# Kernel optimization log

Hardware: AMD Instinct MI355X
Metric: run time of the kernel (lower is better)

## Reference

```python
import jax, jax.numpy as jnp
import numpy as np
from jax import lax

NUM_HEADS = 4
OUT_DIM = 384
HEAD_DIM = 96
STRIDE_Q = 2
STRIDE_KV = 2
EPS = 1e-6
SCALE = HEAD_DIM ** -0.5


def _layernorm(x, g, b):
    m = jnp.mean(x, axis=-1, keepdims=True)
    v = jnp.mean((x - m) ** 2, axis=-1, keepdims=True)
    return (x - m) * lax.rsqrt(v + EPS) * g + b


def _pool(x, w, h, wd, stride):
    # x: [B, nh, N, hd] -> depthwise conv stride-s -> [B, nh, oh*ow, hd]
    B, nh, N, hd = x.shape
    x = x.reshape(B * nh, h, wd, hd).transpose(0, 3, 1, 2)  # NCHW
    y = lax.conv_general_dilated(x, w, (stride, stride), ((1, 1), (1, 1)),
                                 feature_group_count=hd)
    oh, ow = y.shape[2], y.shape[3]
    y = y.reshape(B, nh, hd, oh * ow).transpose(0, 1, 3, 2)
    return y, (oh, ow)


def _add_rel_pos(attn, q, q_size, k_size, rel_h, rel_w):
    qh, qw = q_size
    kh, kw = k_size
    B, nh, _, hd = q.shape
    qhr = max(kh / qh, 1.0); khr = max(qh / kh, 1.0)
    dh = (jnp.arange(qh)[:, None] * qhr - jnp.arange(kh)[None, :] * khr
          + (kh - 1) * khr).astype(jnp.int32)
    qwr = max(kw / qw, 1.0); kwr = max(qw / kw, 1.0)
    dw = (jnp.arange(qw)[:, None] * qwr - jnp.arange(kw)[None, :] * kwr
          + (kw - 1) * kwr).astype(jnp.int32)
    Reh = rel_h[dh]  # [qh, kh, hd]
    Rew = rel_w[dw]  # [qw, kw, hd]
    qr = q.reshape(B, nh, qh, qw, hd)
    eh = jnp.einsum('byhwc,hkc->byhwk', qr, Reh)
    ew = jnp.einsum('byhwc,wkc->byhwk', qr, Rew)
    a = attn.reshape(B, nh, qh, qw, kh, kw) + eh[..., :, None] + ew[..., None, :]
    return a.reshape(B, nh, qh * qw, kh * kw)


def setup_inputs() -> dict:
    key = jax.random.key(0)
    ks = jax.random.split(key, 8)
    B, N, IN_DIM = 16, 3136, 192
    return {
        'hidden_states': jax.random.normal(ks[0], (B, N, IN_DIM), jnp.float32),
        'qkv_w': jax.random.normal(ks[1], (IN_DIM, 3 * OUT_DIM), jnp.float32) * 0.02,
        'qkv_b': jax.random.normal(ks[2], (3 * OUT_DIM,), jnp.float32) * 0.02,
        'pool_q_w': jax.random.normal(ks[3], (HEAD_DIM, 1, 3, 3), jnp.float32) * 0.1,
        'pool_k_w': jax.random.normal(ks[4], (HEAD_DIM, 1, 3, 3), jnp.float32) * 0.1,
        'pool_v_w': jax.random.normal(ks[5], (HEAD_DIM, 1, 3, 3), jnp.float32) * 0.1,
        'ln_q_g': jnp.ones((HEAD_DIM,), jnp.float32),
        'ln_q_b': jnp.zeros((HEAD_DIM,), jnp.float32),
        'ln_k_g': jnp.ones((HEAD_DIM,), jnp.float32),
        'ln_k_b': jnp.zeros((HEAD_DIM,), jnp.float32),
        'ln_v_g': jnp.ones((HEAD_DIM,), jnp.float32),
        'ln_v_b': jnp.zeros((HEAD_DIM,), jnp.float32),
        'rel_h': jax.random.normal(ks[6], (55, HEAD_DIM), jnp.float32) * 0.02,
        'rel_w': jax.random.normal(ks[7], (55, HEAD_DIM), jnp.float32) * 0.02,
        'height': 56,
        'width': 56,
    }


def reference(hidden_states, qkv_w, qkv_b, pool_q_w, pool_k_w, pool_v_w,
              ln_q_g, ln_q_b, ln_k_g, ln_k_b, ln_v_g, ln_v_b,
              rel_h, rel_w, height, width):
    B, N, _ = hidden_states.shape
    qkv = (hidden_states @ qkv_w + qkv_b).reshape(B, N, 3, NUM_HEADS, HEAD_DIM)
    qkv = qkv.transpose(2, 0, 3, 1, 4)  # [3, B, nh, N, hd]
    q, k, v = qkv[0], qkv[1], qkv[2]

    q, q_size = _pool(q, pool_q_w, height, width, STRIDE_Q)
    q = _layernorm(q, ln_q_g, ln_q_b)
    k, k_size = _pool(k, pool_k_w, height, width, STRIDE_KV)
    k = _layernorm(k, ln_k_g, ln_k_b)
    v, _ = _pool(v, pool_v_w, height, width, STRIDE_KV)
    v = _layernorm(v, ln_v_g, ln_v_b)

    attn = jnp.einsum('bhqd,bhkd->bhqk', q * SCALE, k)
    attn = _add_rel_pos(attn, q, q_size, k_size, rel_h, rel_w)
    attn = jax.nn.softmax(attn, axis=-1)
    out = jnp.einsum('bhqk,bhkd->bhqd', attn, v)
    out = out + q  # residual pooling (no cls token)
    out = out.transpose(0, 2, 1, 3).reshape(B, -1, OUT_DIM)
    return out
```

## Files before the change

kernel.cpp:

```cpp
#include <hip/hip_runtime.h>

#define DEVI __device__ __forceinline__

typedef __attribute__((ext_vector_type(8))) short short8;
typedef __attribute__((ext_vector_type(4))) short short4v;
typedef __attribute__((ext_vector_type(4))) float f32x4;
typedef __attribute__((ext_vector_type(4))) unsigned int u32x4;

#define ATTN_SCALE 0.10206207261596575f

DEVI unsigned short f2bf(float f){
  unsigned u = __float_as_uint(f);
  u += 0x7fff + ((u >> 16) & 1);
  return (unsigned short)(u >> 16);
}
DEVI float bf2f(unsigned short h){ return __uint_as_float(((unsigned)h) << 16); }

DEVI void gload16(const void* g, void* l){
  __builtin_amdgcn_global_load_lds((const __attribute__((address_space(1))) void*)g,
                                   (__attribute__((address_space(3))) void*)l, 16, 0, 0);
}

DEVI f32x4 mfma16(short8 a, short8 b, f32x4 c){
  return __builtin_amdgcn_mfma_f32_16x16x32_bf16(a, b, c, 0, 0, 0);
}

DEVI short8 pack_bf8(const float* p){
  float4 a = *(const float4*)p, b = *(const float4*)(p + 4);
  short8 r;
  r[0] = f2bf(a.x); r[1] = f2bf(a.y); r[2] = f2bf(a.z); r[3] = f2bf(a.w);
  r[4] = f2bf(b.x); r[5] = f2bf(b.y); r[6] = f2bf(b.z); r[7] = f2bf(b.w);
  return r;
}

__global__ __launch_bounds__(256) void k_convert(const float4* __restrict__ hs4,
    const float* __restrict__ w, unsigned short* __restrict__ hsb,
    unsigned short* __restrict__ wt){
  const int stride = gridDim.x * 256;
  const int t0 = blockIdx.x * 256 + threadIdx.x;
  const int n4 = (50176 * 192) / 4;
  for (int i = t0; i < n4; i += stride){
    float4 v = hs4[i];
    uint2 p;
    p.x = (unsigned)f2bf(v.x) | ((unsigned)f2bf(v.y) << 16);
    p.y = (unsigned)f2bf(v.z) | ((unsigned)f2bf(v.w) << 16);
    ((uint2*)hsb)[i] = p;
  }
  for (int i = t0; i < 192 * 1152; i += stride){
    int k = i / 1152, n = i - k * 1152;
    wt[n * 192 + k] = f2bf(w[i]);
  }
}

__global__ __launch_bounds__(256) void k_gemm(const unsigned short* __restrict__ A,
    const unsigned short* __restrict__ Bt,
    const float* __restrict__ bias, unsigned short* __restrict__ C){
  __shared__ unsigned short sA[2][128 * 64];
  __shared__ unsigned short sB[2][128 * 64];
  const int bid = (blockIdx.x & 7) * 441 + (blockIdx.x >> 3);
  const int bn = bid % 9, bm = bid / 9;
  const int tid = threadIdx.x, w = tid >> 6, l = tid & 63;
  const int wr = (w >> 1) * 64, wc = (w & 1) * 64;
  const int l15 = l & 15, l4 = l >> 4;
  const f32x4 z4 = {0.f, 0.f, 0.f, 0.f};
  f32x4 acc[4][4];
#pragma unroll
  for (int i = 0; i < 4; ++i)
#pragma unroll
    for (int j = 0; j < 4; ++j) acc[i][j] = z4;

  auto stage = [&](int kk, int buf){
    const int k0 = kk * 64;
#pragma unroll
    for (int i = 0; i < 4; ++i){
      const int ib = (w * 4 + i) << 10;
      const int Lb = ib + (l << 4);
      const int r  = Lb >> 7;
      const int g  = ((Lb >> 4) & 7) ^ (r & 7);
      gload16((const char*)A  + (size_t)(bm * 128 + r) * 384 + k0 * 2 + g * 16, (char*)sA[buf] + ib);
      gload16((const char*)Bt + (size_t)(bn * 128 + r) * 384 + k0 * 2 + g * 16, (char*)sB[buf] + ib);
    }
  };

  stage(0, 0);
  __syncthreads();
  for (int kk = 0; kk < 3; ++kk){
    const int buf = kk & 1;
    if (kk < 2) stage(kk + 1, buf ^ 1);
#pragma unroll
    for (int ks = 0; ks < 2; ++ks){
      short8 av[4], bv[4];
#pragma unroll
      for (int mf = 0; mf < 4; ++mf){
        const int r = wr + mf * 16 + l15;
        const int slot = (ks * 4 + l4) ^ (r & 7);
        av[mf] = *(const short8*)(sA[buf] + r * 64 + slot * 8);
      }
#pragma unroll
      for (int nf = 0; nf < 4; ++nf){
        const int r = wc + nf * 16 + l15;
        const int slot = (ks * 4 + l4) ^ (r & 7);
        bv[nf] = *(const short8*)(sB[buf] + r * 64 + slot * 8);
      }
#pragma unroll
      for (int mf = 0; mf < 4; ++mf)
#pragma unroll
        for (int nf = 0; nf < 4; ++nf)
          acc[mf][nf] = mfma16(av[mf], bv[nf], acc[mf][nf]);
    }
    if (kk < 2) __syncthreads();
  }
#pragma unroll
  for (int nf = 0; nf < 4; ++nf){
    const int col = bn * 128 + wc + nf * 16 + l15;
    const float bv = bias[col];
#pragma unroll
    for (int mf = 0; mf < 4; ++mf)
#pragma unroll
      for (int reg = 0; reg < 4; ++reg){
        const int row = bm * 128 + wr + mf * 16 + l4 * 4 + reg;
        C[(size_t)row * 1152 + col] = f2bf(acc[mf][nf][reg] + bv);
      }
  }
}

__global__ __launch_bounds__(384) void k_pool_ln(const unsigned short* __restrict__ qkv,
    const float* __restrict__ wq, const float* __restrict__ wk, const float* __restrict__ wv,
    const float* __restrict__ gq, const float* __restrict__ bq,
    const float* __restrict__ gk, const float* __restrict__ bk,
    const float* __restrict__ gv, const float* __restrict__ bv,
    unsigned short* __restrict__ qp, unsigned short* __restrict__ kp,
    unsigned short* __restrict__ vpt, float* __restrict__ qpf){
  __shared__ float swt[9 * 96];
  __shared__ float sg[96], sb[96];
  __shared__ float sbuf[28 * 96];
  const int bid = blockIdx.x;
  const int oy = bid % 28, h = (bid / 28) & 3, b = (bid / 112) & 15, which = bid / 1792;
  const float* wsel = which == 0 ? wq : (which == 1 ? wk : wv);
  const float* gsel = which == 0 ? gq : (which == 1 ? gk : gv);
  const float* bsel = which == 0 ? bq : (which == 1 ? bk : bv);
  const int tid = threadIdx.x;
  for (int i = tid; i < 864; i += 384){
    const int d = i / 9, t = i - d * 9;
    swt[t * 96 + d] = wsel[i];
  }
  if (tid < 96){ sg[tid] = gsel[tid]; sb[tid] = bsel[tid]; }
  __syncthreads();

  const int colbase = which * 384 + h * 96;
  if (tid < 336){
    const int ox = tid / 12, d0 = (tid - ox * 12) * 8;
    float acc[8] = {0.f,0.f,0.f,0.f,0.f,0.f,0.f,0.f};
#pragma unroll
    for (int ky = 0; ky < 3; ++ky){
      const int iy = oy * 2 + ky - 1;
      if ((unsigned)iy >= 56u) continue;
      const unsigned short* rowp = qkv + (size_t)(b * 3136 + iy * 56) * 1152 + colbase + d0;
#pragma unroll
      for (int kx = 0; kx < 3; ++kx){
        const int ix = ox * 2 + kx - 1;
        if ((unsigned)ix >= 56u) continue;
        const u32x4 raw = *(const u32x4*)(rowp + (size_t)ix * 1152);
        const float* wv8 = swt + (ky * 3 + kx) * 96 + d0;
        const float4 wa = *(const float4*)wv8;
        const float4 wb = *(const float4*)(wv8 + 4);
        acc[0] += __uint_as_float(raw[0] << 16)         * wa.x;
        acc[1] += __uint_as_float(raw[0] & 0xffff0000u) * wa.y;
        acc[2] += __uint_as_float(raw[1] << 16)         * wa.z;
        acc[3] += __uint_as_float(raw[1] & 0xffff0000u) * wa.w;
        acc[4] += __uint_as_float(raw[2] << 16)         * wb.x;
        acc[5] += __uint_as_float(raw[2] & 0xffff0000u) * wb.y;
        acc[6] += __uint_as_float(raw[3] << 16)         * wb.z;
        acc[7] += __uint_as_float(raw[3] & 0xffff0000u) * wb.w;
      }
    }
    *(float4*)(sbuf + ox * 96 + d0)     = *(float4*)acc;
    *(float4*)(sbuf + ox * 96 + d0 + 4) = *(float4*)(acc + 4);
  }
  __syncthreads();

  const int grp = tid >> 3, l8 = tid & 7;
  if (grp < 28){
    const int ox = grp, d0 = l8 * 12;
    float x[12];
    *(float4*)x       = *(const float4*)(sbuf + ox * 96 + d0);
    *(float4*)(x + 4) = *(const float4*)(sbuf + ox * 96 + d0 + 4);
    *(float4*)(x + 8) = *(const float4*)(sbuf + ox * 96 + d0 + 8);
    float s = 0.f, ss = 0.f;
#pragma unroll
    for (int j = 0; j < 12; ++j){ s += x[j]; ss += x[j] * x[j]; }
#pragma unroll
    for (int d = 1; d < 8; d <<= 1){ s += __shfl_xor(s, d); ss += __shfl_xor(ss, d); }
    const float mean = s * (1.f / 96.f);
    const float var  = ss * (1.f / 96.f) - mean * mean;
    const float rstd = rsqrtf(var + 1e-6f);
    const int n = oy * 28 + ox;
    const size_t bh = (size_t)(b * 4 + h);
    float y[12];
#pragma unroll
    for (int j = 0; j < 12; ++j)
      y[j] = (x[j] - mean) * rstd * sg[d0 + j] + sb[d0 + j];
    if (which == 0){
      const size_t idx = (bh * 784 + n) * 96 + d0;
#pragma unroll
      for (int c = 0; c < 3; ++c){
        short4v p;
        p[0] = (short)f2bf(y[c*4]);   p[1] = (short)f2bf(y[c*4+1]);
        p[2] = (short)f2bf(y[c*4+2]); p[3] = (short)f2bf(y[c*4+3]);
        *(short4v*)(qp + idx + c * 4) = p;
        *(float4*)(qpf + idx + c * 4) = *(const float4*)(y + c * 4);
      }
    } else if (which == 1){
      const size_t idx = (bh * 784 + n) * 96 + d0;
#pragma unroll
      for (int c = 0; c < 3; ++c){
        short4v p;
        p[0] = (short)f2bf(y[c*4]   * ATTN_SCALE); p[1] = (short)f2bf(y[c*4+1] * ATTN_SCALE);
        p[2] = (short)f2bf(y[c*4+2] * ATTN_SCALE); p[3] = (short)f2bf(y[c*4+3] * ATTN_SCALE);
        *(short4v*)(kp + idx + c * 4) = p;
      }
    } else {
#pragma unroll
      for (int j = 0; j < 12; ++j)
        vpt[(bh * 96 + d0 + j) * 784 + n] = f2bf(y[j]);
    }
  }
}

__global__ __launch_bounds__(512, 4) void k_attn(
    const unsigned short* __restrict__ qp, const unsigned short* __restrict__ kp,
    const unsigned short* __restrict__ vpt, const float* __restrict__ qpf,
    const float* __restrict__ relh, const float* __restrict__ relw,
    float* __restrict__ out){
  __shared__ unsigned short sK[2][64 * 128];
  __shared__ unsigned short sV[96 * 64];
  __shared__ unsigned short sP[128 * 64];
  __shared__ unsigned short sGh[128 * 34];
  __shared__ unsigned short sGw[128 * 34];

  const int s = blockIdx.x, xcd = s & 7, slot = s >> 3;
  const int bh = xcd * 8 + slot / 7, qb = slot - (slot / 7) * 7;
  const int b = bh >> 2, h = bh & 3;
  const int tid = threadIdx.x, w = tid >> 6, l = tid & 63;
  const int l15 = l & 15, l4 = l >> 4;
  const size_t base = (size_t)bh * 784 * 96;
  const f32x4 z4 = {0.f, 0.f, 0.f, 0.f};
  const int qrl = w * 16 + l15;
  int q_l = qb * 128 + qrl; if (q_l > 783) q_l = 783;
  const int gbase = qrl * 34;

  auto stageK = [&](int t, int buf){
#pragma unroll
    for (int i = 0; i < 2; ++i){
      const int ib = (w * 2 + i) << 10;
      const int Lb = ib + (l << 4);
      const int r = Lb >> 8;
      const int g = ((Lb >> 4) & 15) ^ (r & 7);
      int kr = t * 64 + r; if (kr > 783) kr = 783;
      const size_t gb = (base + (size_t)kr * 96) * 2 + (g < 12 ? g * 16 : 0);
      gload16((const char*)kp + gb, (char*)sK[buf] + ib);
    }
  };
  short8 vreg[2];
  auto loadV = [&](int t){
    if (tid < 384){
#pragma unroll
      for (int i = 0; i < 2; ++i){
        const int off = (tid * 2 + i) << 4;
        const int r = off >> 7;
        const int g = ((off >> 4) & 7) ^ (r & 7);
        int koff = t * 64 + g * 8; if (koff + 8 > 784) koff = 0;
        vreg[i] = *(const short8*)(vpt + (size_t)(bh * 96 + r) * 784 + koff);
      }
    }
  };
  auto writeV = [&](){
    if (tid < 384){
#pragma unroll
      for (int i = 0; i < 2; ++i)
        *(short8*)((char*)sV + ((tid * 2 + i) << 4)) = vreg[i];
    }
  };

  stageK(0, 0);
  loadV(0);

  short8 qf[3];
#pragma unroll
  for (int ks = 0; ks < 3; ++ks)
    qf[ks] = *(const short8*)(qp + base + (size_t)q_l * 96 + ks * 32 + l4 * 8);

  const int hh = (q_l * 2341) >> 16;
  const int ww = q_l - hh * 28;
  const int h0 = (qb * 128) / 28;

  {
    f32x4 gh[3] = {z4, z4, z4}, gw[4] = {z4, z4, z4, z4};
#pragma unroll
    for (int nf = 0; nf < 3; ++nf){
      int j = h0 + nf * 16 + l15; if (j > 54) j = 54;
#pragma unroll
      for (int ks = 0; ks < 3; ++ks)
        gh[nf] = mfma16(pack_bf8(relh + j * 96 + ks * 32 + l4 * 8), qf[ks], gh[nf]);
    }
#pragma unroll
    for (int nf = 0; nf < 4; ++nf){
      int j = nf * 16 + l15; if (j > 54) j = 54;
#pragma unroll
      for (int ks = 0; ks < 3; ++ks)
        gw[nf] = mfma16(pack_bf8(relw + j * 96 + ks * 32 + l4 * 8), qf[ks], gw[nf]);
    }
#pragma unroll
    for (int nf = 0; nf < 3; ++nf)
#pragma unroll
      for (int reg = 0; reg < 4; ++reg){
        const int j = h0 + nf * 16 + l4 * 4 + reg;
        const int kh = hh + 27 - j;
        if ((unsigned)kh < 28u) sGh[gbase + kh] = f2bf(gh[nf][reg]);
      }
#pragma unroll
    for (int nf = 0; nf < 4; ++nf)
#pragma unroll
      for (int reg = 0; reg < 4; ++reg){
        const int j = nf * 16 + l4 * 4 + reg;
        const int kw = ww + 27 - j;
        if ((unsigned)kw < 28u) sGw[gbase + kw] = f2bf(gw[nf][reg]);
      }
  }

  float m = -1e30f, lsum = 0.f;
  f32x4 acc[6];
#pragma unroll
  for (int i = 0; i < 6; ++i) acc[i] = z4;

  writeV();
  __syncthreads();

  for (int kt = 0; kt < 13; ++kt){
    const int cur = kt & 1;
    if (kt < 12){ loadV(kt + 1); stageK(kt + 1, cur ^ 1); }

    f32x4 sfr[4] = {z4, z4, z4, z4};
#pragma unroll
    for (int ks = 0; ks < 3; ++ks){
#pragma unroll
      for (int nf = 0; nf < 4; ++nf){
        const int r = nf * 16 + l15;
        const int sl = (ks * 4 + l4) ^ (r & 7);
        const short8 kb = *(const short8*)(sK[cur] + r * 128 + sl * 8);
        sfr[nf] = mfma16(kb, qf[ks], sfr[nf]);
      }
    }

#pragma unroll
    for (int nf = 0; nf < 4; ++nf){
      const int kb0 = kt * 64 + nf * 16 + l4 * 4;
#pragma unroll
      for (int reg = 0; reg < 4; ++reg){
        const int k = kb0 + reg;
        const int kh = (k * 2341) >> 16;
        const int kw = k - kh * 28;
        float v = sfr[nf][reg] + bf2f(sGh[gbase + kh]) + bf2f(sGw[gbase + kw]);
        if (k >= 784) v = -1e30f;
        sfr[nf][reg] = v;
      }
    }
    float mx;
    {
      float a0 = fmaxf(fmaxf(sfr[0][0], sfr[0][1]), fmaxf(sfr[0][2], sfr[0][3]));
      float a1 = fmaxf(fmaxf(sfr[1][0], sfr[1][1]), fmaxf(sfr[1][2], sfr[1][3]));
      float a2 = fmaxf(fmaxf(sfr[2][0], sfr[2][1]), fmaxf(sfr[2][2], sfr[2][3]));
      float a3 = fmaxf(fmaxf(sfr[3][0], sfr[3][1]), fmaxf(sfr[3][2], sfr[3][3]));
      mx = fmaxf(fmaxf(a0, a1), fmaxf(a2, a3));
    }
    mx = fmaxf(mx, __shfl_xor(mx, 16));
    mx = fmaxf(mx, __shfl_xor(mx, 32));
    const float mn = fmaxf(m, mx);
    const float al = __expf(m - mn);
    m = mn;
    float sum;
    {
#pragma unroll
      for (int nf = 0; nf < 4; ++nf)
#pragma unroll
        for (int reg = 0; reg < 4; ++reg)
          sfr[nf][reg] = __expf(sfr[nf][reg] - mn);
      float s0 = (sfr[0][0] + sfr[0][1]) + (sfr[0][2] + sfr[0][3]);
      float s1 = (sfr[1][0] + sfr[1][1]) + (sfr[1][2] + sfr[1][3]);
      float s2 = (sfr[2][0] + sfr[2][1]) + (sfr[2][2] + sfr[2][3]);
      float s3 = (sfr[3][0] + sfr[3][1]) + (sfr[3][2] + sfr[3][3]);
      sum = (s0 + s1) + (s2 + s3);
    }
    sum += __shfl_xor(sum, 16);
    sum += __shfl_xor(sum, 32);
    lsum = lsum * al + sum;

#pragma unroll
    for (int nf = 0; nf < 4; ++nf){
      short4v p4;
      p4[0] = (short)f2bf(sfr[nf][0]); p4[1] = (short)f2bf(sfr[nf][1]);
      p4[2] = (short)f2bf(sfr[nf][2]); p4[3] = (short)f2bf(sfr[nf][3]);
      char* dst = (char*)sP + qrl * 128 + (((nf * 2 + (l4 >> 1)) ^ (l15 & 7)) << 4) + ((l4 & 1) << 3);
      *(short4v*)dst = p4;
    }
#pragma unroll
    for (int i = 0; i < 6; ++i)
#pragma unroll
      for (int reg = 0; reg < 4; ++reg)
        acc[i][reg] *= al;

#pragma unroll
    for (int ks = 0; ks < 2; ++ks){
      const short8 pb = *(const short8*)((char*)sP + qrl * 128 + (((ks * 4 + l4) ^ (l15 & 7)) << 4));
#pragma unroll
      for (int nf = 0; nf < 6; ++nf){
        const int r = nf * 16 + l15;
        const int sl = (ks * 4 + l4) ^ (r & 7);
        const short8 vb = *(const short8*)(sV + r * 64 + sl * 8);
        acc[nf] = mfma16(vb, pb, acc[nf]);
      }
    }

    if (kt < 12){
      __syncthreads();
      writeV();
      __syncthreads();
    }
  }

  const int qg = qb * 128 + qrl;
  if (qg < 784){
    const float rcp = 1.f / lsum;
    const float* qrow = qpf + base + (size_t)qg * 96;
    float* orow = out + ((size_t)b * 784 + qg) * 384 + h * 96;
#pragma unroll
    for (int nf = 0; nf < 6; ++nf)
#pragma unroll
      for (int reg = 0; reg < 4; ++reg){
        const int d = nf * 16 + l4 * 4 + reg;
        orow[d] = acc[nf][reg] * rcp + qrow[d];
      }
  }
}

extern "C" void kernel_launch(void* const* d_in, const int* in_sizes, int n_in,
                              void* d_out, int out_size, void* d_ws, size_t ws_size,
                              hipStream_t stream){
  const float* hs  = (const float*)d_in[0];
  const float* qw  = (const float*)d_in[1];
  const float* qb  = (const float*)d_in[2];
  const float* pwq = (const float*)d_in[3];
  const float* pwk = (const float*)d_in[4];
  const float* pwv = (const float*)d_in[5];
  const float* gq  = (const float*)d_in[6];
  const float* bq  = (const float*)d_in[7];
  const float* gk  = (const float*)d_in[8];
  const float* bk  = (const float*)d_in[9];
  const float* gv  = (const float*)d_in[10];
  const float* bv  = (const float*)d_in[11];
  const float* rh  = (const float*)d_in[12];
  const float* rw  = (const float*)d_in[13];
  float* out = (float*)d_out;

  char* ws = (char*)d_ws;
  size_t off = 0;
  auto take = [&](size_t n)->char*{ char* p = ws + off; off += (n + 255) & ~(size_t)255; return p; };
  unsigned short* hsb = (unsigned short*)take((size_t)50176 * 192 * 2);
  unsigned short* wtb = (unsigned short*)take((size_t)1152 * 192 * 2);
  unsigned short* qkv = (unsigned short*)take((size_t)50176 * 1152 * 2);
  unsigned short* qpb = (unsigned short*)take((size_t)64 * 784 * 96 * 2);
  unsigned short* kpb = (unsigned short*)take((size_t)64 * 784 * 96 * 2);
  unsigned short* vpt = (unsigned short*)take((size_t)64 * 784 * 96 * 2);
  float* qpf          = (float*)take((size_t)64 * 784 * 96 * 4);

  hipLaunchKernelGGL(k_convert, dim3(1024), dim3(256), 0, stream,
                     (const float4*)hs, qw, hsb, wtb);
  hipLaunchKernelGGL(k_gemm, dim3(392 * 9), dim3(256), 0, stream, hsb, wtb, qb, qkv);
  hipLaunchKernelGGL(k_pool_ln, dim3(5376), dim3(384), 0, stream, qkv,
                     pwq, pwk, pwv, gq, bq, gk, bk, gv, bv, qpb, kpb, vpt, qpf);
  hipLaunchKernelGGL(k_attn, dim3(448), dim3(512), 0, stream,
                     qpb, kpb, vpt, qpf, rh, rw, out);
}
```

Before: 272.1 us.

## Fold relative-position bias into QK MFMA via one-hot key augmentation

Keys are extended from 96 to 160 columns with one-hot indicators for their row and column. Queries gain two extra k-slices holding their rel-h and rel-w bias rows, so the bias add becomes two extra MFMA k-steps instead of per-element LDS gathers. The softmax moves to exp2 with log2e folded into the K scale and the rel tables. LDS for the bias and P buffers is aliased into the K double buffer, which adds a barrier per tile and raises K global traffic and staging cost.

```diff
diff --git a/kernel.cpp b/kernel.cpp
--- a/kernel.cpp
+++ b/kernel.cpp
@@ -8,6 +8,8 @@
 typedef __attribute__((ext_vector_type(4))) unsigned int u32x4;
 
 #define ATTN_SCALE 0.10206207261596575f
+#define LOG2E      1.4426950408889634f
+#define KSCALE     (ATTN_SCALE * LOG2E)
 
 DEVI unsigned short f2bf(float f){
   unsigned u = __float_as_uint(f);
@@ -25,11 +27,11 @@
   return __builtin_amdgcn_mfma_f32_16x16x32_bf16(a, b, c, 0, 0, 0);
 }
 
-DEVI short8 pack_bf8(const float* p){
+DEVI short8 pack_bf8s(const float* p, float s){
   float4 a = *(const float4*)p, b = *(const float4*)(p + 4);
   short8 r;
-  r[0] = f2bf(a.x); r[1] = f2bf(a.y); r[2] = f2bf(a.z); r[3] = f2bf(a.w);
-  r[4] = f2bf(b.x); r[5] = f2bf(b.y); r[6] = f2bf(b.z); r[7] = f2bf(b.w);
+  r[0] = f2bf(a.x * s); r[1] = f2bf(a.y * s); r[2] = f2bf(a.z * s); r[3] = f2bf(a.w * s);
+  r[4] = f2bf(b.x * s); r[5] = f2bf(b.y * s); r[6] = f2bf(b.z * s); r[7] = f2bf(b.w * s);
   return r;
 }
 
@@ -211,14 +213,24 @@
         *(float4*)(qpf + idx + c * 4) = *(const float4*)(y + c * 4);
       }
     } else if (which == 1){
-      const size_t idx = (bh * 784 + n) * 96 + d0;
+      const size_t idx = (bh * 784 + n) * 160;
 #pragma unroll
       for (int c = 0; c < 3; ++c){
         short4v p;
-        p[0] = (short)f2bf(y[c*4]   * ATTN_SCALE); p[1] = (short)f2bf(y[c*4+1] * ATTN_SCALE);
-        p[2] = (short)f2bf(y[c*4+2] * ATTN_SCALE); p[3] = (short)f2bf(y[c*4+3] * ATTN_SCALE);
-        *(short4v*)(kp + idx + c * 4) = p;
-      }
+        p[0] = (short)f2bf(y[c*4]   * KSCALE); p[1] = (short)f2bf(y[c*4+1] * KSCALE);
+        p[2] = (short)f2bf(y[c*4+2] * KSCALE); p[3] = (short)f2bf(y[c*4+3] * KSCALE);
+        *(short4v*)(kp + idx + d0 + c * 4) = p;
+      }
+      short8 oh;
+#pragma unroll
+      for (int jj = 0; jj < 8; ++jj){
+        const int pcol = 96 + l8 * 8 + jj;
+        unsigned short v = 0;
+        if (pcol == 96 + oy)  v = 0x3F80;
+        if (pcol == 128 + ox) v = 0x3F80;
+        oh[jj] = (short)v;
+      }
+      *(short8*)(kp + idx + 96 + l8 * 8) = oh;
     } else {
 #pragma unroll
       for (int j = 0; j < 12; ++j)
@@ -232,33 +244,31 @@
     const unsigned short* __restrict__ vpt, const float* __restrict__ qpf,
     const float* __restrict__ relh, const float* __restrict__ relw,
     float* __restrict__ out){
-  __shared__ unsigned short sK[2][64 * 128];
+  __shared__ unsigned short sK[2][64 * 160];
   __shared__ unsigned short sV[96 * 64];
-  __shared__ unsigned short sP[128 * 64];
-  __shared__ unsigned short sGh[128 * 34];
-  __shared__ unsigned short sGw[128 * 34];
 
   const int s = blockIdx.x, xcd = s & 7, slot = s >> 3;
   const int bh = xcd * 8 + slot / 7, qb = slot - (slot / 7) * 7;
   const int b = bh >> 2, h = bh & 3;
   const int tid = threadIdx.x, w = tid >> 6, l = tid & 63;
   const int l15 = l & 15, l4 = l >> 4;
-  const size_t base = (size_t)bh * 784 * 96;
+  const size_t baseq = (size_t)bh * 784 * 96;
+  const size_t basek = (size_t)bh * 784 * 160;
   const f32x4 z4 = {0.f, 0.f, 0.f, 0.f};
   const int qrl = w * 16 + l15;
   int q_l = qb * 128 + qrl; if (q_l > 783) q_l = 783;
-  const int gbase = qrl * 34;
 
   auto stageK = [&](int t, int buf){
 #pragma unroll
-    for (int i = 0; i < 2; ++i){
-      const int ib = (w * 2 + i) << 10;
-      const int Lb = ib + (l << 4);
-      const int r = Lb >> 8;
-      const int g = ((Lb >> 4) & 15) ^ (r & 7);
-      int kr = t * 64 + r; if (kr > 783) kr = 783;
-      const size_t gb = (base + (size_t)kr * 96) * 2 + (g < 12 ? g * 16 : 0);
-      gload16((const char*)kp + gb, (char*)sK[buf] + ib);
+    for (int r = 0; r < 3; ++r){
+      if (r == 2 && tid >= 256) continue;
+      const int off = r * 8192 + (tid << 4);
+      const int row = ((off >> 6) * 205) >> 10;
+      const int rem = off - row * 320;
+      const int sg_ = (rem >> 4) ^ (row & 3);
+      int kr = t * 64 + row; if (kr > 783) kr = 783;
+      gload16((const char*)kp + ((size_t)(basek + (size_t)kr * 160) + sg_ * 8) * 2,
+              (char*)sK[buf] + off);
     }
   };
   short8 vreg[2];
@@ -285,30 +295,36 @@
   stageK(0, 0);
   loadV(0);
 
-  short8 qf[3];
+  short8 qf[5];
 #pragma unroll
   for (int ks = 0; ks < 3; ++ks)
-    qf[ks] = *(const short8*)(qp + base + (size_t)q_l * 96 + ks * 32 + l4 * 8);
+    qf[ks] = *(const short8*)(qp + baseq + (size_t)q_l * 96 + ks * 32 + l4 * 8);
 
   const int hh = (q_l * 2341) >> 16;
   const int ww = q_l - hh * 28;
   const int h0 = (qb * 128) / 28;
 
   {
+    unsigned short* sGh = sK[1];
+    unsigned short* sGw = sK[1] + 4096;
     f32x4 gh[3] = {z4, z4, z4}, gw[4] = {z4, z4, z4, z4};
 #pragma unroll
     for (int nf = 0; nf < 3; ++nf){
       int j = h0 + nf * 16 + l15; if (j > 54) j = 54;
 #pragma unroll
       for (int ks = 0; ks < 3; ++ks)
-        gh[nf] = mfma16(pack_bf8(relh + j * 96 + ks * 32 + l4 * 8), qf[ks], gh[nf]);
+        gh[nf] = mfma16(pack_bf8s(relh + j * 96 + ks * 32 + l4 * 8, LOG2E), qf[ks], gh[nf]);
     }
 #pragma unroll
     for (int nf = 0; nf < 4; ++nf){
       int j = nf * 16 + l15; if (j > 54) j = 54;
 #pragma unroll
       for (int ks = 0; ks < 3; ++ks)
-        gw[nf] = mfma16(pack_bf8(relw + j * 96 + ks * 32 + l4 * 8), qf[ks], gw[nf]);
+        gw[nf] = mfma16(pack_bf8s(relw + j * 96 + ks * 32 + l4 * 8, LOG2E), qf[ks], gw[nf]);
+    }
+    if (l4 == 0){
+      *(short4v*)(sGh + qrl * 32 + 28) = (short4v)0;
+      *(short4v*)(sGw + qrl * 32 + 28) = (short4v)0;
     }
 #pragma unroll
     for (int nf = 0; nf < 3; ++nf)
@@ -316,7 +332,7 @@
       for (int reg = 0; reg < 4; ++reg){
         const int j = h0 + nf * 16 + l4 * 4 + reg;
         const int kh = hh + 27 - j;
-        if ((unsigned)kh < 28u) sGh[gbase + kh] = f2bf(gh[nf][reg]);
+        if ((unsigned)kh < 28u) sGh[qrl * 32 + kh] = f2bf(gh[nf][reg]);
       }
 #pragma unroll
     for (int nf = 0; nf < 4; ++nf)
@@ -324,8 +340,10 @@
       for (int reg = 0; reg < 4; ++reg){
         const int j = nf * 16 + l4 * 4 + reg;
         const int kw = ww + 27 - j;
-        if ((unsigned)kw < 28u) sGw[gbase + kw] = f2bf(gw[nf][reg]);
-      }
+        if ((unsigned)kw < 28u) sGw[qrl * 32 + kw] = f2bf(gw[nf][reg]);
+      }
+    qf[3] = *(const short8*)(sGh + qrl * 32 + l4 * 8);
+    qf[4] = *(const short8*)(sGw + qrl * 32 + l4 * 8);
   }
 
   float m = -1e30f, lsum = 0.f;
@@ -342,29 +360,20 @@
 
     f32x4 sfr[4] = {z4, z4, z4, z4};
 #pragma unroll
-    for (int ks = 0; ks < 3; ++ks){
+    for (int ks = 0; ks < 5; ++ks){
 #pragma unroll
       for (int nf = 0; nf < 4; ++nf){
         const int r = nf * 16 + l15;
-        const int sl = (ks * 4 + l4) ^ (r & 7);
-        const short8 kb = *(const short8*)(sK[cur] + r * 128 + sl * 8);
+        const int sl = (ks * 4 + l4) ^ (r & 3);
+        const short8 kb = *(const short8*)(sK[cur] + r * 160 + sl * 8);
         sfr[nf] = mfma16(kb, qf[ks], sfr[nf]);
       }
     }
-
-#pragma unroll
-    for (int nf = 0; nf < 4; ++nf){
-      const int kb0 = kt * 64 + nf * 16 + l4 * 4;
-#pragma unroll
-      for (int reg = 0; reg < 4; ++reg){
-        const int k = kb0 + reg;
-        const int kh = (k * 2341) >> 16;
-        const int kw = k - kh * 28;
-        float v = sfr[nf][reg] + bf2f(sGh[gbase + kh]) + bf2f(sGw[gbase + kw]);
-        if (k >= 784) v = -1e30f;
-        sfr[nf][reg] = v;
-      }
-    }
+    if (kt == 12){
+      const f32x4 m30 = {-1e30f, -1e30f, -1e30f, -1e30f};
+      sfr[1] = m30; sfr[2] = m30; sfr[3] = m30;
+    }
+
     float mx;
     {
       float a0 = fmaxf(fmaxf(sfr[0][0], sfr[0][1]), fmaxf(sfr[0][2], sfr[0][3]));
@@ -376,7 +385,7 @@
     mx = fmaxf(mx, __shfl_xor(mx, 16));
     mx = fmaxf(mx, __shfl_xor(mx, 32));
     const float mn = fmaxf(m, mx);
-    const float al = __expf(m - mn);
+    const float al = exp2f(m - mn);
     m = mn;
     float sum;
     {
@@ -384,7 +393,7 @@
       for (int nf = 0; nf < 4; ++nf)
 #pragma unroll
         for (int reg = 0; reg < 4; ++reg)
-          sfr[nf][reg] = __expf(sfr[nf][reg] - mn);
+          sfr[nf][reg] = exp2f(sfr[nf][reg] - mn);
       float s0 = (sfr[0][0] + sfr[0][1]) + (sfr[0][2] + sfr[0][3]);
       float s1 = (sfr[1][0] + sfr[1][1]) + (sfr[1][2] + sfr[1][3]);
       float s2 = (sfr[2][0] + sfr[2][1]) + (sfr[2][2] + sfr[2][3]);
@@ -395,12 +404,15 @@
     sum += __shfl_xor(sum, 32);
     lsum = lsum * al + sum;
 
+    __syncthreads();
+
+    unsigned short* sPp = sK[cur];
 #pragma unroll
     for (int nf = 0; nf < 4; ++nf){
       short4v p4;
       p4[0] = (short)f2bf(sfr[nf][0]); p4[1] = (short)f2bf(sfr[nf][1]);
       p4[2] = (short)f2bf(sfr[nf][2]); p4[3] = (short)f2bf(sfr[nf][3]);
-      char* dst = (char*)sP + qrl * 128 + (((nf * 2 + (l4 >> 1)) ^ (l15 & 7)) << 4) + ((l4 & 1) << 3);
+      char* dst = (char*)sPp + qrl * 128 + (((nf * 2 + (l4 >> 1)) ^ (l15 & 7)) << 4) + ((l4 & 1) << 3);
       *(short4v*)dst = p4;
     }
 #pragma unroll
@@ -411,7 +423,7 @@
 
 #pragma unroll
     for (int ks = 0; ks < 2; ++ks){
-      const short8 pb = *(const short8*)((char*)sP + qrl * 128 + (((ks * 4 + l4) ^ (l15 & 7)) << 4));
+      const short8 pb = *(const short8*)((char*)sPp + qrl * 128 + (((ks * 4 + l4) ^ (l15 & 7)) << 4));
 #pragma unroll
       for (int nf = 0; nf < 6; ++nf){
         const int r = nf * 16 + l15;
@@ -431,7 +443,7 @@
   const int qg = qb * 128 + qrl;
   if (qg < 784){
     const float rcp = 1.f / lsum;
-    const float* qrow = qpf + base + (size_t)qg * 96;
+    const float* qrow = qpf + baseq + (size_t)qg * 96;
     float* orow = out + ((size_t)b * 784 + qg) * 384 + h * 96;
 #pragma unroll
     for (int nf = 0; nf < 6; ++nf)
@@ -469,7 +481,7 @@
   unsigned short* wtb = (unsigned short*)take((size_t)1152 * 192 * 2);
   unsigned short* qkv = (unsigned short*)take((size_t)50176 * 1152 * 2);
   unsigned short* qpb = (unsigned short*)take((size_t)64 * 784 * 96 * 2);
-  unsigned short* kpb = (unsigned short*)take((size_t)64 * 784 * 96 * 2);
+  unsigned short* kpb = (unsigned short*)take((size_t)64 * 784 * 160 * 2);
   unsigned short* vpt = (unsigned short*)take((size_t)64 * 784 * 96 * 2);
   float* qpf          = (float*)take((size_t)64 * 784 * 96 * 4);
 
```

New measurement: 269.8 us. Within noise of the previous version (-0.8%).
